# Performance work log

Hardware: AMD Instinct MI355X
Metric: run time of the kernel (lower is better)

Reference implementation:

```python
import jax, jax.numpy as jnp
import numpy as np

N_CLASSES = 5
N_SAMPLES = 512
D_EMB = 512


def setup_inputs() -> dict:
    key = jax.random.key(0)
    k1, k2, k3 = jax.random.split(key, 3)
    prediction = jax.random.normal(k1, (N_SAMPLES, D_EMB), dtype=jnp.float32)
    target = jax.random.randint(k2, (N_SAMPLES,), 0, N_CLASSES)
    # learnable_map=None -> all learnable, init = inverse_softplus(0.5 + 0.5*U[0,1))
    t = 0.5 + 0.5 * jax.random.uniform(k3, (N_CLASSES - 1,), dtype=jnp.float32)
    distances_raw = jnp.log(jnp.exp(t) - 1.0)  # inverse softplus (t < 20 always)
    return {"prediction": prediction, "distances_raw": distances_raw, "target": target}


def reference(prediction, distances_raw, target):
    n = prediction.shape[0]
    eps = 1e-8  # torch F.cosine_similarity eps
    xn = prediction / jnp.maximum(jnp.linalg.norm(prediction, axis=1, keepdims=True), eps)
    cos = xn @ xn.T  # [i, j] pairwise cosine similarity

    same = target[:, None] == target[None, :]          # label_diff <= 0
    positives = same & ~jnp.eye(n, dtype=bool)          # same label, not self
    negatives = ~same                                   # different label

    # ordinal class positions from softplus-parameterized gaps
    pos_d = jax.nn.softplus(distances_raw)
    class_pos = jnp.concatenate([jnp.zeros(1, dtype=pos_d.dtype), jnp.cumsum(pos_d)])
    cp = class_pos[target]
    margins = jnp.where(negatives, jnp.abs(cp[:, None] - cp[None, :]), 0.0)  # [i, j]

    # Original loop over anchor-positive columns k:
    #   n_pair_loss[k][i, j] = -cos[i, k] + cos[i, j] + margins[i, j]
    #   valid iff positives[i, k] and negatives[i, j]; invalid -> relu(-inf)=0
    base = cos + margins                                # [i, j]
    diff = base[:, None, :] - cos[:, :, None]           # [i, k, j]
    val = jnp.where(negatives[:, None, :], jax.nn.relu(diff), 0.0)
    s = jnp.where(positives, val.sum(axis=2), 0.0)      # [i, k]
    negcount = negatives.sum(axis=1)                    # [i]
    cnt = jnp.where(positives, negcount[:, None], 0)    # loss_mask2
    L = s / jnp.maximum(cnt, 1)                         # per (anchor i, positive k)

    # mean over nonzero entries (mean_n_pair_loss[mean_n_pair_loss != 0].mean())
    nz = (L != 0.0).sum()
    return L.sum() / jnp.maximum(nz, 1).astype(L.dtype)
```

## Files before the change

### kernel.cpp

```cpp
#include <hip/hip_runtime.h>
#include <math.h>

#define NS 512
#define DE 512
#define NCL 5
#define NBLK 256


__global__ __launch_bounds__(512) void k_all(const float* __restrict__ pred,
                                             const int* __restrict__ target,
                                             const float* __restrict__ draw,
                                             unsigned int* __restrict__ ctrl,
                                             float* __restrict__ out) {
    const int b = blockIdx.x;
    const int tid = threadIdx.x;
    const int iA = b, iB = b + 256;

    __shared__ float  rn_s[NS];
    __shared__ float  ckA[NS], ckB[NS];
    __shared__ float4 v4sA[NS / 4], v4sB[NS / 4];
    __shared__ int    pkA[NS], pkB[NS];
    __shared__ float  spart[NS * 17];
    __shared__ float  redf[512];
    __shared__ int    redi[512];
    __shared__ unsigned int pcA, pcB;

    float* gsum = (float*)ctrl;
    unsigned int* gnz    = ctrl + 1;
    unsigned int* ticket = ctrl + 2;

    if (tid == 0) { pcA = 0u; pcB = 0u; }

    const int w = tid >> 6, lane = tid & 63;
    const int g = lane >> 4, s = lane & 15;

    const float4* pA = (const float4*)&pred[(size_t)iA * DE];
    const float4* pB = (const float4*)&pred[(size_t)iB * DE];
    float4 fA[8], fB[8];
#pragma unroll
    for (int p = 0; p < 8; p++) { fA[p] = pA[p * 16 + s]; fB[p] = pB[p * 16 + s]; }

#pragma unroll 4
    for (int t = 0; t < 16; t++) {
        const int j = w * 64 + t * 4 + g;
        const float4* rj = (const float4*)&pred[(size_t)j * DE];
        float aA = 0.0f, aB = 0.0f, aS = 0.0f;
#pragma unroll
        for (int p = 0; p < 8; p++) {
            float4 x = rj[p * 16 + s];
            aA = fmaf(x.x, fA[p].x, aA); aA = fmaf(x.y, fA[p].y, aA);
            aA = fmaf(x.z, fA[p].z, aA); aA = fmaf(x.w, fA[p].w, aA);
            aB = fmaf(x.x, fB[p].x, aB); aB = fmaf(x.y, fB[p].y, aB);
            aB = fmaf(x.z, fB[p].z, aB); aB = fmaf(x.w, fB[p].w, aB);
            aS = fmaf(x.x, x.x, aS);     aS = fmaf(x.y, x.y, aS);
            aS = fmaf(x.z, x.z, aS);     aS = fmaf(x.w, x.w, aS);
        }
#pragma unroll
        for (int m = 1; m <= 8; m <<= 1) {
            aA += __shfl_xor(aA, m);
            aB += __shfl_xor(aB, m);
            aS += __shfl_xor(aS, m);
        }
        if (s == 0) {
            ckA[j] = aA;
            ckB[j] = aB;
            rn_s[j] = 1.0f / fmaxf(sqrtf(aS), 1e-8f);
        }
    }

    float cp[NCL];
    cp[0] = 0.0f;
#pragma unroll
    for (int c = 0; c < NCL - 1; c++) cp[c + 1] = cp[c] + log1pf(expf(draw[c]));
    const int tiA = target[iA], tiB = target[iB];
    const float cpA = cp[tiA], cpB = cp[tiB];
    const int j = tid;
    const int tj = target[j];
    const float cpj = cp[tj];
    __syncthreads();

    const float rniA = rn_s[iA], rniB = rn_s[iB], rnj = rn_s[j];
    {
        float c0 = ckA[j] * rniA * rnj;
        bool n0 = (tj != tiA);
        ckA[j] = c0;
        ((float*)v4sA)[j] = n0 ? (c0 + fabsf(cpA - cpj)) : -1e30f;
        if (!n0 && j != iA) pkA[atomicAdd(&pcA, 1u)] = j;
        redi[tid] = (n0 ? 1 : 0);
    }
    {
        float c0 = ckB[j] * rniB * rnj;
        bool n0 = (tj != tiB);
        ckB[j] = c0;
        ((float*)v4sB)[j] = n0 ? (c0 + fabsf(cpB - cpj)) : -1e30f;
        if (!n0 && j != iB) pkB[atomicAdd(&pcB, 1u)] = j;
        redi[tid] += (n0 ? 1 : 0) << 16;
    }
    __syncthreads();
    for (int s2 = 256; s2 > 0; s2 >>= 1) {
        if (tid < s2) redi[tid] += redi[tid + s2];
        __syncthreads();
    }
    const int negA = redi[0] & 0xffff;
    const int negB = redi[0] >> 16;
    const unsigned int nposA = pcA, nposB = pcB;
    __syncthreads();

    const int kl = tid & 31, jc = tid >> 5;
    const float denA = (float)(negA > 1 ? negA : 1);
    const float denB = (float)(negB > 1 ? negB : 1);
    float contrib = 0.0f;
    int nzc = 0;

    {
        float4 vj[8];
#pragma unroll
        for (int t = 0; t < 8; t++) vj[t] = v4sA[jc * 8 + t];
        for (unsigned int p = kl; p < nposA; p += 32) {
            const float ckp = ckA[pkA[p]];
            float s0 = 0.0f, s1 = 0.0f;
#pragma unroll
            for (int t = 0; t < 8; t++) {
                float4 wv = vj[t];
                s0 += fmaxf(wv.x - ckp, 0.0f) + fmaxf(wv.y - ckp, 0.0f);
                s1 += fmaxf(wv.z - ckp, 0.0f) + fmaxf(wv.w - ckp, 0.0f);
            }
            spart[p * 17 + jc] = s0 + s1;
        }
        __syncthreads();
        for (unsigned int p = tid; p < nposA; p += 512) {
            float s0 = 0.0f;
#pragma unroll
            for (int q = 0; q < 16; q++) s0 += spart[p * 17 + q];
            contrib += s0 / denA;
            if (s0 != 0.0f) nzc++;
        }
        __syncthreads();
    }
    {
        float4 vj[8];
#pragma unroll
        for (int t = 0; t < 8; t++) vj[t] = v4sB[jc * 8 + t];
        for (unsigned int p = kl; p < nposB; p += 32) {
            const float ckp = ckB[pkB[p]];
            float s0 = 0.0f, s1 = 0.0f;
#pragma unroll
            for (int t = 0; t < 8; t++) {
                float4 wv = vj[t];
                s0 += fmaxf(wv.x - ckp, 0.0f) + fmaxf(wv.y - ckp, 0.0f);
                s1 += fmaxf(wv.z - ckp, 0.0f) + fmaxf(wv.w - ckp, 0.0f);
            }
            spart[p * 17 + jc] = s0 + s1;
        }
        __syncthreads();
        for (unsigned int p = tid; p < nposB; p += 512) {
            float s0 = 0.0f;
#pragma unroll
            for (int q = 0; q < 16; q++) s0 += spart[p * 17 + q];
            contrib += s0 / denB;
            if (s0 != 0.0f) nzc++;
        }
    }

    redf[tid] = contrib;
    redi[tid] = nzc;
    __syncthreads();
    for (int s2 = 256; s2 > 0; s2 >>= 1) {
        if (tid < s2) { redf[tid] += redf[tid + s2]; redi[tid] += redi[tid + s2]; }
        __syncthreads();
    }
    if (tid == 0) {
        if (redf[0] != 0.0f || redi[0] != 0) {
            atomicAdd(gsum, redf[0]);
            atomicAdd(gnz, (unsigned int)redi[0]);
        }
        __threadfence();
        unsigned int t = atomicAdd(ticket, 1u);
        if (t == (unsigned int)(NBLK - 1)) {
            float s0 = atomicAdd(gsum, 0.0f);
            unsigned int n = atomicAdd(gnz, 0u);
            out[0] = s0 / (float)(n > 1u ? n : 1u);
        }
    }
}

extern "C" void kernel_launch(void* const* d_in, const int* in_sizes, int n_in,
                              void* d_out, int out_size, void* d_ws, size_t ws_size,
                              hipStream_t stream) {
    const float* pred   = (const float*)d_in[0];
    const float* draw   = (const float*)d_in[1];
    const int*   target = (const int*)d_in[2];
    float* out = (float*)d_out;

    unsigned int* ctrl = (unsigned int*)d_ws;

    hipMemsetAsync(ctrl, 0, 4 * sizeof(unsigned int), stream);
    hipLaunchKernelGGL(k_all, dim3(NBLK), dim3(512), 0, stream,
                       pred, target, draw, ctrl, out);
}
```

Before: 86.84 us.

## Split fused kernel into dot-product and loss kernels via workspace

Splits the single fused kernel into a dot-product kernel with launch bounds allowing two blocks per CU, plus a loss kernel that reads the dots and norms from a global workspace. The dot kernel loads all eight float4 vectors of each row before the FMAs, which raises memory-level parallelism. The aim is to free the GEMV phase from the large shared-memory footprint of the loss phase so it gets higher occupancy. The cost is an extra launch and a round trip of about 1 MB through global memory.

New measurement: 87.73 us. No clear change (+1.0%).

```diff
diff --git a/kernel.cpp b/kernel.cpp
--- a/kernel.cpp
+++ b/kernel.cpp
@@ -7,11 +7,61 @@
 #define NBLK 256
 
 
-__global__ __launch_bounds__(512) void k_all(const float* __restrict__ pred,
-                                             const int* __restrict__ target,
-                                             const float* __restrict__ draw,
-                                             unsigned int* __restrict__ ctrl,
-                                             float* __restrict__ out) {
+__global__ __launch_bounds__(512, 2) void k_dots(const float* __restrict__ pred,
+                                                 float* __restrict__ dotA,
+                                                 float* __restrict__ dotB,
+                                                 float* __restrict__ dg) {
+    const int b = blockIdx.x;
+    const int tid = threadIdx.x;
+    const int iA = b, iB = b + 256;
+
+    const int w = tid >> 6, lane = tid & 63;
+    const int g = lane >> 4, s = lane & 15;
+
+    const float4* pA = (const float4*)&pred[(size_t)iA * DE];
+    const float4* pB = (const float4*)&pred[(size_t)iB * DE];
+    float4 fA[8], fB[8];
+#pragma unroll
+    for (int p = 0; p < 8; p++) { fA[p] = pA[p * 16 + s]; fB[p] = pB[p * 16 + s]; }
+
+#pragma unroll 4
+    for (int t = 0; t < 16; t++) {
+        const int j = w * 64 + t * 4 + g;
+        const float4* rj = (const float4*)&pred[(size_t)j * DE];
+        float4 x[8];
+#pragma unroll
+        for (int p = 0; p < 8; p++) x[p] = rj[p * 16 + s];
+        float aA = 0.0f, aB = 0.0f, aS = 0.0f;
+#pragma unroll
+        for (int p = 0; p < 8; p++) {
+            aA = fmaf(x[p].x, fA[p].x, aA); aA = fmaf(x[p].y, fA[p].y, aA);
+            aA = fmaf(x[p].z, fA[p].z, aA); aA = fmaf(x[p].w, fA[p].w, aA);
+            aB = fmaf(x[p].x, fB[p].x, aB); aB = fmaf(x[p].y, fB[p].y, aB);
+            aB = fmaf(x[p].z, fB[p].z, aB); aB = fmaf(x[p].w, fB[p].w, aB);
+            aS = fmaf(x[p].x, x[p].x, aS);  aS = fmaf(x[p].y, x[p].y, aS);
+            aS = fmaf(x[p].z, x[p].z, aS);  aS = fmaf(x[p].w, x[p].w, aS);
+        }
+#pragma unroll
+        for (int m = 1; m <= 8; m <<= 1) {
+            aA += __shfl_xor(aA, m);
+            aB += __shfl_xor(aB, m);
+            aS += __shfl_xor(aS, m);
+        }
+        if (s == 0) {
+            dotA[(size_t)b * NS + j] = aA;
+            dotB[(size_t)b * NS + j] = aB;
+            if (b == 0) dg[j] = aS;
+        }
+    }
+}
+
+__global__ __launch_bounds__(512) void k_loss(const float* __restrict__ dotA,
+                                              const float* __restrict__ dotB,
+                                              const float* __restrict__ dg,
+                                              const int* __restrict__ target,
+                                              const float* __restrict__ draw,
+                                              unsigned int* __restrict__ ctrl,
+                                              float* __restrict__ out) {
     const int b = blockIdx.x;
     const int tid = threadIdx.x;
     const int iA = b, iB = b + 256;
@@ -31,42 +81,12 @@
 
     if (tid == 0) { pcA = 0u; pcB = 0u; }
 
-    const int w = tid >> 6, lane = tid & 63;
-    const int g = lane >> 4, s = lane & 15;
-
-    const float4* pA = (const float4*)&pred[(size_t)iA * DE];
-    const float4* pB = (const float4*)&pred[(size_t)iB * DE];
-    float4 fA[8], fB[8];
-#pragma unroll
-    for (int p = 0; p < 8; p++) { fA[p] = pA[p * 16 + s]; fB[p] = pB[p * 16 + s]; }
-
-#pragma unroll 4
-    for (int t = 0; t < 16; t++) {
-        const int j = w * 64 + t * 4 + g;
-        const float4* rj = (const float4*)&pred[(size_t)j * DE];
-        float aA = 0.0f, aB = 0.0f, aS = 0.0f;
-#pragma unroll
-        for (int p = 0; p < 8; p++) {
-            float4 x = rj[p * 16 + s];
-            aA = fmaf(x.x, fA[p].x, aA); aA = fmaf(x.y, fA[p].y, aA);
-            aA = fmaf(x.z, fA[p].z, aA); aA = fmaf(x.w, fA[p].w, aA);
-            aB = fmaf(x.x, fB[p].x, aB); aB = fmaf(x.y, fB[p].y, aB);
-            aB = fmaf(x.z, fB[p].z, aB); aB = fmaf(x.w, fB[p].w, aB);
-            aS = fmaf(x.x, x.x, aS);     aS = fmaf(x.y, x.y, aS);
-            aS = fmaf(x.z, x.z, aS);     aS = fmaf(x.w, x.w, aS);
-        }
-#pragma unroll
-        for (int m = 1; m <= 8; m <<= 1) {
-            aA += __shfl_xor(aA, m);
-            aB += __shfl_xor(aB, m);
-            aS += __shfl_xor(aS, m);
-        }
-        if (s == 0) {
-            ckA[j] = aA;
-            ckB[j] = aB;
-            rn_s[j] = 1.0f / fmaxf(sqrtf(aS), 1e-8f);
-        }
-    }
+    const int j = tid;
+    const float da = dotA[(size_t)b * NS + j];
+    const float db = dotB[(size_t)b * NS + j];
+    const float ns = dg[j];
+    const float rnj = 1.0f / fmaxf(sqrtf(ns), 1e-8f);
+    rn_s[j] = rnj;
 
     float cp[NCL];
     cp[0] = 0.0f;
@@ -74,14 +94,13 @@
     for (int c = 0; c < NCL - 1; c++) cp[c + 1] = cp[c] + log1pf(expf(draw[c]));
     const int tiA = target[iA], tiB = target[iB];
     const float cpA = cp[tiA], cpB = cp[tiB];
-    const int j = tid;
     const int tj = target[j];
     const float cpj = cp[tj];
     __syncthreads();
 
-    const float rniA = rn_s[iA], rniB = rn_s[iB], rnj = rn_s[j];
-    {
-        float c0 = ckA[j] * rniA * rnj;
+    const float rniA = rn_s[iA], rniB = rn_s[iB];
+    {
+        float c0 = da * rniA * rnj;
         bool n0 = (tj != tiA);
         ckA[j] = c0;
         ((float*)v4sA)[j] = n0 ? (c0 + fabsf(cpA - cpj)) : -1e30f;
@@ -89,7 +108,7 @@
         redi[tid] = (n0 ? 1 : 0);
     }
     {
-        float c0 = ckB[j] * rniB * rnj;
+        float c0 = db * rniB * rnj;
         bool n0 = (tj != tiB);
         ckB[j] = c0;
         ((float*)v4sB)[j] = n0 ? (c0 + fabsf(cpB - cpj)) : -1e30f;
@@ -192,9 +211,14 @@
     const int*   target = (const int*)d_in[2];
     float* out = (float*)d_out;
 
-    unsigned int* ctrl = (unsigned int*)d_ws;
+    float* ws   = (float*)d_ws;
+    float* dotA = ws;
+    float* dotB = ws + NBLK * NS;
+    float* dg   = ws + 2 * NBLK * NS;
+    unsigned int* ctrl = (unsigned int*)(dg + NS);
 
     hipMemsetAsync(ctrl, 0, 4 * sizeof(unsigned int), stream);
-    hipLaunchKernelGGL(k_all, dim3(NBLK), dim3(512), 0, stream,
-                       pred, target, draw, ctrl, out);
+    hipLaunchKernelGGL(k_dots, dim3(NBLK), dim3(512), 0, stream, pred, dotA, dotB, dg);
+    hipLaunchKernelGGL(k_loss, dim3(NBLK), dim3(512), 0, stream,
+                       dotA, dotB, dg, target, draw, ctrl, out);
 }
```
